# Performance work log

Measured on AMD Instinct MI355X. Metric: run time of the kernel, lower is better.

The kernel has to match this reference:

```python
import jax, jax.numpy as jnp
import numpy as np

G, T, D_IN, D_OUT = 8, 8192, 1024, 1024
# fixed uneven per-expert token counts summing to T (variable-size groups)
_COUNTS = np.array([512, 1536, 1024, 1024, 768, 1280, 896, 1152], dtype=np.int32)
assert _COUNTS.sum() == T


def setup_inputs() -> dict:
    key = jax.random.key(0)
    k1, k2 = jax.random.split(key)
    hidden_states = jax.random.normal(k1, (T, D_IN), dtype=jnp.float32)
    # kaiming_uniform_(a=sqrt(5)) on [G, in, out] -> bound = sqrt(3/ (fan_in)) with gain sqrt(1/3)
    bound = 1.0 / np.sqrt(D_IN)
    weight = jax.random.uniform(k2, (G, D_IN, D_OUT), dtype=jnp.float32, minval=-bound, maxval=bound)
    tokens_per_expert = jnp.asarray(_COUNTS)
    return {"hidden_states": hidden_states, "weight": weight, "tokens_per_expert": tokens_per_expert}


def reference(hidden_states, weight, tokens_per_expert):
    # grouped GEMM: token t in group g (per contiguous split by tokens_per_expert)
    # gets out[t] = hidden_states[t] @ weight[g]
    T_ = hidden_states.shape[0]
    G_ = weight.shape[0]
    offsets = jnp.cumsum(tokens_per_expert)  # [G] end offsets of each group
    expert_id = jnp.searchsorted(offsets, jnp.arange(T_), side="right")  # [T]
    out = jnp.zeros((T_, weight.shape[2]), dtype=hidden_states.dtype)
    for g in range(G_):  # small fixed expert count; masked accumulate keeps shapes static
        mask = (expert_id == g).astype(hidden_states.dtype)[:, None]
        out = out + mask * (hidden_states @ weight[g])
    return out
```

## Files before the change

### kernel.cpp

```cpp
#include <hip/hip_runtime.h>
#include <hip/hip_bf16.h>
#include <stdint.h>

typedef __attribute__((ext_vector_type(8))) short short8;
typedef __attribute__((ext_vector_type(4))) float f32x4;

constexpr int Tt = 8192, Kd = 1024, Nd = 1024, Gn = 8;
constexpr int BM = 128, BN = 256, BK = 64;
constexpr int NKT = Kd / BK;

static __device__ __forceinline__ short f2bf(float x) {
    __hip_bfloat16 b = __float2bfloat16(x);
    return *reinterpret_cast<short*>(&b);
}

__global__ __launch_bounds__(512, 2)
void grouped_gemm_kernel(const float* __restrict__ H,
                         const float* __restrict__ W,
                         const int* __restrict__ counts,
                         float* __restrict__ out)
{
    __shared__ __align__(16) short As[2][BM * BK];
    __shared__ __align__(16) short Bs[2][BN * BK];

    const int tid = threadIdx.x;
    const int bid = blockIdx.x;
    const int swz = (bid & 7) * 32 + (bid >> 3);
    const int mt = swz >> 2, nt = swz & 3;
    const int row0 = mt * BM, col0 = nt * BN;

    int g = 0;
    {
        int c = 0;
        for (int i = 0; i < Gn; ++i) { c += counts[i]; if (row0 >= c) g = i + 1; }
    }
    const float* __restrict__ Wg = W + (size_t)g * Kd * Nd;

    const int wid = tid >> 6, lane = tid & 63;
    const int wm = wid >> 2, wn = wid & 3;
    const int l15 = lane & 15, l4 = lane >> 4;

    const int ra = tid >> 2, ca = tid & 3;
    const int nb = tid & 255, kh = tid >> 8;

    f32x4 acc[4][4];
#pragma unroll
    for (int i = 0; i < 4; ++i)
#pragma unroll
        for (int j = 0; j < 4; ++j) acc[i][j] = (f32x4)0.0f;

    f32x4 av[4];
    float bv[32];

    auto load_a = [&](int kt) {
        const float* p = H + (size_t)(row0 + ra) * Kd + kt * BK + ca * 16;
#pragma unroll
        for (int j = 0; j < 4; ++j) av[j] = *(const f32x4*)(p + j * 4);
    };
    auto load_b = [&](int kt) {
        const float* p = Wg + (size_t)(kt * BK + kh * 32) * Nd + col0 + nb;
#pragma unroll
        for (int j = 0; j < 32; ++j) bv[j] = p[(size_t)j * Nd];
    };
    auto write_a = [&](int buf) {
        short8 v0, v1;
#pragma unroll
        for (int j = 0; j < 4; ++j) {
            v0[j] = f2bf(av[0][j]); v0[4 + j] = f2bf(av[1][j]);
            v1[j] = f2bf(av[2][j]); v1[4 + j] = f2bf(av[3][j]);
        }
        const int s = ra & 7;
        *(short8*)&As[buf][ra * 64 + (((ca * 2) ^ s) << 3)] = v0;
        *(short8*)&As[buf][ra * 64 + (((ca * 2 + 1) ^ s) << 3)] = v1;
    };
    auto write_b = [&](int buf) {
        const int s = nb & 7;
#pragma unroll
        for (int c = 0; c < 4; ++c) {
            short8 v;
#pragma unroll
            for (int j = 0; j < 8; ++j) v[j] = f2bf(bv[c * 8 + j]);
            *(short8*)&Bs[buf][nb * 64 + (((kh * 4 + c) ^ s) << 3)] = v;
        }
    };

    auto rd_a = [&](int buf, int mi, int ks) -> short8 {
        const int m = wm * 64 + mi * 16 + l15;
        return *(const short8*)&As[buf][m * 64 + (((ks * 4 + l4) ^ (m & 7)) << 3)];
    };
    auto rd_b = [&](int buf, int ni, int ks) -> short8 {
        const int n = wn * 64 + ni * 16 + l15;
        return *(const short8*)&Bs[buf][n * 64 + (((ks * 4 + l4) ^ (n & 7)) << 3)];
    };

    load_a(0); load_b(0);
    write_a(0); write_b(0);
    asm volatile("s_waitcnt lgkmcnt(0)" ::: "memory");
    __builtin_amdgcn_s_barrier();

    int buf = 0;
    for (int kt = 0; kt < NKT; ++kt) {
        const bool more = (kt + 1 < NKT);
        if (more) { load_a(kt + 1); load_b(kt + 1); }

        short8 a0[2][2], a1[2][2], b0[2][2], b1[2][2];

#pragma unroll
        for (int i = 0; i < 2; ++i)
#pragma unroll
            for (int ks = 0; ks < 2; ++ks) { a0[i][ks] = rd_a(buf, i, ks); b0[i][ks] = rd_b(buf, i, ks); }
        __builtin_amdgcn_s_setprio(1);
#pragma unroll
        for (int mi = 0; mi < 2; ++mi)
#pragma unroll
            for (int ni = 0; ni < 2; ++ni)
#pragma unroll
                for (int ks = 0; ks < 2; ++ks)
                    acc[mi][ni] = __builtin_amdgcn_mfma_f32_16x16x32_bf16(
                        a0[mi][ks], b0[ni][ks], acc[mi][ni], 0, 0, 0);
        __builtin_amdgcn_s_setprio(0);

#pragma unroll
        for (int i = 0; i < 2; ++i)
#pragma unroll
            for (int ks = 0; ks < 2; ++ks) a1[i][ks] = rd_a(buf, 2 + i, ks);
        __builtin_amdgcn_s_setprio(1);
#pragma unroll
        for (int mi = 0; mi < 2; ++mi)
#pragma unroll
            for (int ni = 0; ni < 2; ++ni)
#pragma unroll
                for (int ks = 0; ks < 2; ++ks)
                    acc[2 + mi][ni] = __builtin_amdgcn_mfma_f32_16x16x32_bf16(
                        a1[mi][ks], b0[ni][ks], acc[2 + mi][ni], 0, 0, 0);
        __builtin_amdgcn_s_setprio(0);

        if (more) { write_a(buf ^ 1); write_b(buf ^ 1); }

#pragma unroll
        for (int i = 0; i < 2; ++i)
#pragma unroll
            for (int ks = 0; ks < 2; ++ks) b1[i][ks] = rd_b(buf, 2 + i, ks);
        __builtin_amdgcn_s_setprio(1);
#pragma unroll
        for (int mi = 0; mi < 2; ++mi)
#pragma unroll
            for (int ni = 0; ni < 2; ++ni)
#pragma unroll
                for (int ks = 0; ks < 2; ++ks)
                    acc[2 + mi][2 + ni] = __builtin_amdgcn_mfma_f32_16x16x32_bf16(
                        a1[mi][ks], b1[ni][ks], acc[2 + mi][2 + ni], 0, 0, 0);
        __builtin_amdgcn_s_setprio(0);

        __builtin_amdgcn_s_setprio(1);
#pragma unroll
        for (int mi = 0; mi < 2; ++mi)
#pragma unroll
            for (int ni = 0; ni < 2; ++ni)
#pragma unroll
                for (int ks = 0; ks < 2; ++ks)
                    acc[mi][2 + ni] = __builtin_amdgcn_mfma_f32_16x16x32_bf16(
                        a0[mi][ks], b1[ni][ks], acc[mi][2 + ni], 0, 0, 0);
        __builtin_amdgcn_s_setprio(0);

        asm volatile("s_waitcnt lgkmcnt(0)" ::: "memory");
        __builtin_amdgcn_s_barrier();
        buf ^= 1;
    }

#pragma unroll
    for (int mi = 0; mi < 4; ++mi) {
        const int rbase = row0 + wm * 64 + mi * 16 + l4 * 4;
#pragma unroll
        for (int ni = 0; ni < 4; ++ni) {
            const int c = col0 + wn * 64 + ni * 16 + l15;
#pragma unroll
            for (int r = 0; r < 4; ++r)
                out[(size_t)(rbase + r) * Nd + c] = acc[mi][ni][r];
        }
    }
}

extern "C" void kernel_launch(void* const* d_in, const int* in_sizes, int n_in,
                              void* d_out, int out_size, void* d_ws, size_t ws_size,
                              hipStream_t stream) {
    const float* H = (const float*)d_in[0];
    const float* W = (const float*)d_in[1];
    const int* counts = (const int*)d_in[2];
    float* out = (float*)d_out;
    const int grid = (Tt / BM) * (Nd / BN);
    grouped_gemm_kernel<<<grid, 512, 0, stream>>>(H, W, counts, out);
}
```

Before: 39.22 us.

## Pre-convert inputs to bf16 and stream tiles via direct global-to-LDS loads

Adds a prep kernel that converts hidden states to bf16 and transposes and converts the expert weights into a workspace. The main GEMM then loads tiles with global_load_lds straight into LDS, using a three-stage buffer ring and vmcnt-based waits instead of per-thread register loads, conversion and LDS stores. This takes the strided fp32 weight loads and the in-loop conversion out of the GEMM's critical path. In exchange it adds an extra kernel launch that reads and writes about 48 MB, which may cost more than it saves. A fallback to the old fp32 path runs when the workspace is too small.

Measured after the change: 47.48 us. 21.1% more time.

```diff
diff --git a/kernel.cpp b/kernel.cpp
--- a/kernel.cpp
+++ b/kernel.cpp
@@ -3,6 +3,7 @@
 #include <stdint.h>
 
 typedef __attribute__((ext_vector_type(8))) short short8;
+typedef __attribute__((ext_vector_type(4))) short short4s;
 typedef __attribute__((ext_vector_type(4))) float f32x4;
 
 constexpr int Tt = 8192, Kd = 1024, Nd = 1024, Gn = 8;
@@ -14,14 +15,57 @@
     return *reinterpret_cast<short*>(&b);
 }
 
+__global__ __launch_bounds__(256)
+void prep_kernel(const float* __restrict__ H, const float* __restrict__ W,
+                 short* __restrict__ Hb, short* __restrict__ Wt)
+{
+    const int b = blockIdx.x, t = threadIdx.x;
+    if (b < 2048) {
+        const int g = b >> 8, r = b & 255;
+        const int kb = (r >> 4) * 64, nb = (r & 15) * 64;
+        const float* src = W + (size_t)g * Kd * Nd + (size_t)kb * Nd + nb;
+        __shared__ float Ls[64 * 64];
+#pragma unroll
+        for (int i = 0; i < 4; ++i) {
+            const int s = i * 256 + t;
+            const int k = s >> 4, gc = s & 15;
+            const f32x4 v = *(const f32x4*)(src + (size_t)k * Nd + ((gc ^ (k & 15)) << 2));
+            *(f32x4*)&Ls[k * 64 + (gc << 2)] = v;
+        }
+        __syncthreads();
+        short* dst = Wt + (size_t)g * Nd * Kd + (size_t)nb * Kd + kb;
+#pragma unroll
+        for (int i = 0; i < 2; ++i) {
+            const int s = i * 256 + t;
+            const int n = s >> 3, kc = s & 7;
+            short8 v;
+#pragma unroll
+            for (int j = 0; j < 8; ++j) {
+                const int k = kc * 8 + j;
+                v[j] = f2bf(Ls[k * 64 + ((((n >> 2) ^ (k & 15)) << 2) | (n & 3))]);
+            }
+            *(short8*)(dst + (size_t)n * Kd + kc * 8) = v;
+        }
+    } else {
+        const int hb = b - 2048;
+#pragma unroll
+        for (int i = 0; i < 8; ++i) {
+            const size_t gidx = (size_t)i * 262144 + (size_t)hb * 256 + t;
+            const f32x4 x = *(const f32x4*)(H + gidx * 4);
+            short4s v;
+#pragma unroll
+            for (int j = 0; j < 4; ++j) v[j] = f2bf(x[j]);
+            *(short4s*)(Hb + gidx * 4) = v;
+        }
+    }
+}
+
 __global__ __launch_bounds__(512, 2)
-void grouped_gemm_kernel(const float* __restrict__ H,
-                         const float* __restrict__ W,
-                         const int* __restrict__ counts,
-                         float* __restrict__ out)
+void gemm_bf16_kernel(const short* __restrict__ Hb, const short* __restrict__ Wt,
+                      const int* __restrict__ counts, float* __restrict__ out)
 {
-    __shared__ __align__(16) short As[2][BM * BK];
-    __shared__ __align__(16) short Bs[2][BN * BK];
+    __shared__ __align__(16) short As[3][BM * BK];
+    __shared__ __align__(16) short Bs[3][BN * BK];
 
     const int tid = threadIdx.x;
     const int bid = blockIdx.x;
@@ -34,24 +78,124 @@
         int c = 0;
         for (int i = 0; i < Gn; ++i) { c += counts[i]; if (row0 >= c) g = i + 1; }
     }
-    const float* __restrict__ Wg = W + (size_t)g * Kd * Nd;
+    const short* __restrict__ Wg = Wt + (size_t)g * Nd * Kd;
 
     const int wid = tid >> 6, lane = tid & 63;
     const int wm = wid >> 2, wn = wid & 3;
     const int l15 = lane & 15, l4 = lane >> 4;
 
+    f32x4 acc[4][4];
+#pragma unroll
+    for (int i = 0; i < 4; ++i)
+#pragma unroll
+        for (int j = 0; j < 4; ++j) acc[i][j] = (f32x4)0.0f;
+
+    auto stage = [&](int kt, int buf) {
+#pragma unroll
+        for (int i = 0; i < 2; ++i) {
+            const int q = i * 8 + wid;
+            const int s = q * 64 + lane;
+            const int row = s >> 3, gc = (s & 7) ^ (row & 7);
+            const short* src = Hb + (size_t)(row0 + row) * Kd + kt * BK + gc * 8;
+            __builtin_amdgcn_global_load_lds(
+                (const __attribute__((address_space(1))) uint32_t*)src,
+                (__attribute__((address_space(3))) uint32_t*)(&As[buf][q * 512]),
+                16, 0, 0);
+        }
+#pragma unroll
+        for (int i = 0; i < 4; ++i) {
+            const int q = i * 8 + wid;
+            const int s = q * 64 + lane;
+            const int row = s >> 3, gc = (s & 7) ^ (row & 7);
+            const short* src = Wg + (size_t)(col0 + row) * Kd + kt * BK + gc * 8;
+            __builtin_amdgcn_global_load_lds(
+                (const __attribute__((address_space(1))) uint32_t*)src,
+                (__attribute__((address_space(3))) uint32_t*)(&Bs[buf][q * 512]),
+                16, 0, 0);
+        }
+    };
+
+    auto compute = [&](int buf) {
+#pragma unroll
+        for (int ks = 0; ks < 2; ++ks) {
+            short8 af[4], bf[4];
+#pragma unroll
+            for (int mi = 0; mi < 4; ++mi) {
+                const int m = wm * 64 + mi * 16 + l15;
+                af[mi] = *(const short8*)&As[buf][m * 64 + (((ks * 4 + l4) ^ (m & 7)) << 3)];
+            }
+#pragma unroll
+            for (int ni = 0; ni < 4; ++ni) {
+                const int n = wn * 64 + ni * 16 + l15;
+                bf[ni] = *(const short8*)&Bs[buf][n * 64 + (((ks * 4 + l4) ^ (n & 7)) << 3)];
+            }
+            __builtin_amdgcn_s_setprio(1);
+#pragma unroll
+            for (int mi = 0; mi < 4; ++mi)
+#pragma unroll
+                for (int ni = 0; ni < 4; ++ni)
+                    acc[mi][ni] = __builtin_amdgcn_mfma_f32_16x16x32_bf16(
+                        af[mi], bf[ni], acc[mi][ni], 0, 0, 0);
+            __builtin_amdgcn_s_setprio(0);
+        }
+    };
+
+    stage(0, 0);
+    stage(1, 1);
+    asm volatile("s_waitcnt vmcnt(6)" ::: "memory");
+    __builtin_amdgcn_s_barrier();
+    __builtin_amdgcn_sched_barrier(0);
+
+    int b0 = 0, bs = 2;
+    for (int kt = 0; kt < NKT; ++kt) {
+        if (kt + 2 < NKT) stage(kt + 2, bs);
+        compute(b0);
+        if (kt + 1 < NKT) {
+            if (kt + 2 < NKT) asm volatile("s_waitcnt vmcnt(6)" ::: "memory");
+            else              asm volatile("s_waitcnt vmcnt(0)" ::: "memory");
+            __builtin_amdgcn_s_barrier();
+            __builtin_amdgcn_sched_barrier(0);
+        }
+        b0 = (b0 == 2) ? 0 : b0 + 1;
+        bs = (bs == 2) ? 0 : bs + 1;
+    }
+
+#pragma unroll
+    for (int mi = 0; mi < 4; ++mi) {
+        const int rbase = row0 + wm * 64 + mi * 16 + l4 * 4;
+#pragma unroll
+        for (int ni = 0; ni < 4; ++ni) {
+            const int c = col0 + wn * 64 + ni * 16 + l15;
+#pragma unroll
+            for (int r = 0; r < 4; ++r)
+                out[(size_t)(rbase + r) * Nd + c] = acc[mi][ni][r];
+        }
+    }
+}
+
+__global__ __launch_bounds__(512, 2)
+void gemm_f32_fallback(const float* __restrict__ H, const float* __restrict__ W,
+                       const int* __restrict__ counts, float* __restrict__ out)
+{
+    __shared__ __align__(16) short As[2][BM * BK];
+    __shared__ __align__(16) short Bs2[2][BN * BK];
+    const int tid = threadIdx.x, bid = blockIdx.x;
+    const int swz = (bid & 7) * 32 + (bid >> 3);
+    const int mt = swz >> 2, nt = swz & 3;
+    const int row0 = mt * BM, col0 = nt * BN;
+    int g = 0; { int c = 0; for (int i = 0; i < Gn; ++i) { c += counts[i]; if (row0 >= c) g = i + 1; } }
+    const float* __restrict__ Wg = W + (size_t)g * Kd * Nd;
+    const int wid = tid >> 6, lane = tid & 63;
+    const int wm = wid >> 2, wn = wid & 3;
+    const int l15 = lane & 15, l4 = lane >> 4;
     const int ra = tid >> 2, ca = tid & 3;
     const int nb = tid & 255, kh = tid >> 8;
-
     f32x4 acc[4][4];
 #pragma unroll
     for (int i = 0; i < 4; ++i)
 #pragma unroll
         for (int j = 0; j < 4; ++j) acc[i][j] = (f32x4)0.0f;
-
-    f32x4 av[4];
-    float bv[32];
-
+    f32x4 av[4]; float bv[32];
     auto load_a = [&](int kt) {
         const float* p = H + (size_t)(row0 + ra) * Kd + kt * BK + ca * 16;
 #pragma unroll
@@ -80,94 +224,42 @@
             short8 v;
 #pragma unroll
             for (int j = 0; j < 8; ++j) v[j] = f2bf(bv[c * 8 + j]);
-            *(short8*)&Bs[buf][nb * 64 + (((kh * 4 + c) ^ s) << 3)] = v;
-        }
-    };
-
-    auto rd_a = [&](int buf, int mi, int ks) -> short8 {
-        const int m = wm * 64 + mi * 16 + l15;
-        return *(const short8*)&As[buf][m * 64 + (((ks * 4 + l4) ^ (m & 7)) << 3)];
-    };
-    auto rd_b = [&](int buf, int ni, int ks) -> short8 {
-        const int n = wn * 64 + ni * 16 + l15;
-        return *(const short8*)&Bs[buf][n * 64 + (((ks * 4 + l4) ^ (n & 7)) << 3)];
-    };
-
-    load_a(0); load_b(0);
-    write_a(0); write_b(0);
-    asm volatile("s_waitcnt lgkmcnt(0)" ::: "memory");
-    __builtin_amdgcn_s_barrier();
-
+            *(short8*)&Bs2[buf][nb * 64 + (((kh * 4 + c) ^ s) << 3)] = v;
+        }
+    };
+    auto compute = [&](int buf) {
+#pragma unroll
+        for (int ks = 0; ks < 2; ++ks) {
+            short8 af[4], bf[4];
+#pragma unroll
+            for (int mi = 0; mi < 4; ++mi) {
+                const int m = wm * 64 + mi * 16 + l15;
+                af[mi] = *(const short8*)&As[buf][m * 64 + (((ks * 4 + l4) ^ (m & 7)) << 3)];
+            }
+#pragma unroll
+            for (int ni = 0; ni < 4; ++ni) {
+                const int n = wn * 64 + ni * 16 + l15;
+                bf[ni] = *(const short8*)&Bs2[buf][n * 64 + (((ks * 4 + l4) ^ (n & 7)) << 3)];
+            }
+#pragma unroll
+            for (int mi = 0; mi < 4; ++mi)
+#pragma unroll
+                for (int ni = 0; ni < 4; ++ni)
+                    acc[mi][ni] = __builtin_amdgcn_mfma_f32_16x16x32_bf16(
+                        af[mi], bf[ni], acc[mi][ni], 0, 0, 0);
+        }
+    };
+    load_a(0); load_b(0); write_a(0); write_b(0);
+    __syncthreads();
     int buf = 0;
     for (int kt = 0; kt < NKT; ++kt) {
         const bool more = (kt + 1 < NKT);
         if (more) { load_a(kt + 1); load_b(kt + 1); }
-
-        short8 a0[2][2], a1[2][2], b0[2][2], b1[2][2];
-
-#pragma unroll
-        for (int i = 0; i < 2; ++i)
-#pragma unroll
-            for (int ks = 0; ks < 2; ++ks) { a0[i][ks] = rd_a(buf, i, ks); b0[i][ks] = rd_b(buf, i, ks); }
-        __builtin_amdgcn_s_setprio(1);
-#pragma unroll
-        for (int mi = 0; mi < 2; ++mi)
-#pragma unroll
-            for (int ni = 0; ni < 2; ++ni)
-#pragma unroll
-                for (int ks = 0; ks < 2; ++ks)
-                    acc[mi][ni] = __builtin_amdgcn_mfma_f32_16x16x32_bf16(
-                        a0[mi][ks], b0[ni][ks], acc[mi][ni], 0, 0, 0);
-        __builtin_amdgcn_s_setprio(0);
-
-#pragma unroll
-        for (int i = 0; i < 2; ++i)
-#pragma unroll
-            for (int ks = 0; ks < 2; ++ks) a1[i][ks] = rd_a(buf, 2 + i, ks);
-        __builtin_amdgcn_s_setprio(1);
-#pragma unroll
-        for (int mi = 0; mi < 2; ++mi)
-#pragma unroll
-            for (int ni = 0; ni < 2; ++ni)
-#pragma unroll
-                for (int ks = 0; ks < 2; ++ks)
-                    acc[2 + mi][ni] = __builtin_amdgcn_mfma_f32_16x16x32_bf16(
-                        a1[mi][ks], b0[ni][ks], acc[2 + mi][ni], 0, 0, 0);
-        __builtin_amdgcn_s_setprio(0);
-
+        compute(buf);
         if (more) { write_a(buf ^ 1); write_b(buf ^ 1); }
-
-#pragma unroll
-        for (int i = 0; i < 2; ++i)
-#pragma unroll
-            for (int ks = 0; ks < 2; ++ks) b1[i][ks] = rd_b(buf, 2 + i, ks);
-        __builtin_amdgcn_s_setprio(1);
-#pragma unroll
-        for (int mi = 0; mi < 2; ++mi)
-#pragma unroll
-            for (int ni = 0; ni < 2; ++ni)
-#pragma unroll
-                for (int ks = 0; ks < 2; ++ks)
-                    acc[2 + mi][2 + ni] = __builtin_amdgcn_mfma_f32_16x16x32_bf16(
-                        a1[mi][ks], b1[ni][ks], acc[2 + mi][2 + ni], 0, 0, 0);
-        __builtin_amdgcn_s_setprio(0);
-
-        __builtin_amdgcn_s_setprio(1);
-#pragma unroll
-        for (int mi = 0; mi < 2; ++mi)
-#pragma unroll
-            for (int ni = 0; ni < 2; ++ni)
-#pragma unroll
-                for (int ks = 0; ks < 2; ++ks)
-                    acc[mi][2 + ni] = __builtin_amdgcn_mfma_f32_16x16x32_bf16(
-                        a0[mi][ks], b1[ni][ks], acc[mi][2 + ni], 0, 0, 0);
-        __builtin_amdgcn_s_setprio(0);
-
-        asm volatile("s_waitcnt lgkmcnt(0)" ::: "memory");
-        __builtin_amdgcn_s_barrier();
+        __syncthreads();
         buf ^= 1;
     }
-
 #pragma unroll
     for (int mi = 0; mi < 4; ++mi) {
         const int rbase = row0 + wm * 64 + mi * 16 + l4 * 4;
@@ -188,6 +280,13 @@
     const float* W = (const float*)d_in[1];
     const int* counts = (const int*)d_in[2];
     float* out = (float*)d_out;
-    const int grid = (Tt / BM) * (Nd / BN);
-    grouped_gemm_kernel<<<grid, 512, 0, stream>>>(H, W, counts, out);
-}
+    const size_t need = (size_t)(Tt * Kd + Gn * Kd * Nd) * sizeof(short);
+    if (ws_size >= need) {
+        short* Hb = (short*)d_ws;
+        short* Wt = Hb + (size_t)Tt * Kd;
+        prep_kernel<<<3072, 256, 0, stream>>>(H, W, Hb, Wt);
+        gemm_bf16_kernel<<<256, 512, 0, stream>>>(Hb, Wt, counts, out);
+    } else {
+        gemm_f32_fallback<<<256, 512, 0, stream>>>(H, W, counts, out);
+    }
+}
```
